# Optimization experiments

Measured on AMD Instinct MI355X. Metric: run time of the kernel, lower is better.

## Reference

```python
import jax, jax.numpy as jnp
import numpy as np

D_LOW = 32
LAGS = [1, 2, 4, 8]
# Upper-triangular pair indices (offset=1), matching torch.triu_indices(d_low, d_low, 1)
IDX_I, IDX_J = np.triu_indices(D_LOW, k=1)
IDX_I = jnp.asarray(IDX_I)
IDX_J = jnp.asarray(IDX_J)
EPS = 1e-6


def setup_inputs() -> dict:
    key = jax.random.key(0)
    ks = jax.random.split(key, 7)
    b, n, d_model = 4, 4096, 1024
    d_plucker = D_LOW * (D_LOW - 1) // 2  # 496
    s = lambda fan_in: 1.0 / np.sqrt(fan_in)
    return {
        "x": jax.random.normal(ks[0], (b, n, d_model), dtype=jnp.float32),
        "W_red": jax.random.normal(ks[1], (d_model, D_LOW), dtype=jnp.float32) * s(d_model),
        "b_red": jax.random.normal(ks[2], (D_LOW,), dtype=jnp.float32) * s(d_model),
        "W_exp": jax.random.normal(ks[3], (d_plucker, d_model), dtype=jnp.float32) * s(d_plucker),
        "b_exp": jax.random.normal(ks[4], (d_model,), dtype=jnp.float32) * s(d_plucker),
        "W_gate": jax.random.normal(ks[5], (2 * d_model, d_model), dtype=jnp.float32) * s(2 * d_model),
        "b_gate": jax.random.normal(ks[6], (d_model,), dtype=jnp.float32) * s(2 * d_model),
    }


def reference(x, W_red, b_red, W_exp, b_exp, W_gate, b_gate):
    b, n, _ = x.shape
    d_plucker = D_LOW * (D_LOW - 1) // 2
    z = x @ W_red + b_red  # [b, n, d_low]
    plucker_total = jnp.zeros((b, n, d_plucker), dtype=x.dtype)
    counts = jnp.zeros((b, n, 1), dtype=x.dtype)
    for lag in LAGS:
        if lag <= 0 or lag >= n:
            continue
        z_curr = z[:, lag:, :]   # [b, n-lag, d_low]
        z_past = z[:, :-lag, :]  # [b, n-lag, d_low]
        # Antisymmetric Plucker coordinates over upper-triangular index pairs
        p = (z_curr[:, :, IDX_I] * z_past[:, :, IDX_J]
             - z_curr[:, :, IDX_J] * z_past[:, :, IDX_I])  # [b, n-lag, d_plucker]
        norm = jnp.linalg.norm(p, axis=-1, keepdims=True)
        p = p / jnp.maximum(norm, EPS)
        plucker_total = plucker_total.at[:, lag:, :].add(p)
        counts = counts.at[:, lag:, :].add(1.0)
    counts = jnp.maximum(counts, 1.0)
    plucker_avg = plucker_total / counts
    g_avg = plucker_avg @ W_exp + b_exp  # [b, n, d_model]
    concat = jnp.concatenate([x, g_avg], axis=-1)  # [b, n, 2*d_model]
    gate = jax.nn.sigmoid(concat @ W_gate + b_gate)
    return gate * x + (1.0 - gate) * g_avg
```

## Files before the change

kernel.cpp:

```cpp
#include <hip/hip_runtime.h>
#include <hip/hip_bf16.h>
#include <math.h>

#define B_DIM   4
#define N_DIM   4096
#define D_MODEL 1024
#define D_LOW   32
#define NPAIR   496
#define NROWS   (B_DIM * N_DIM)
#define KPAD3   512
#define LDA2    1536

typedef __bf16 bf16;
typedef __bf16 bf16x8 __attribute__((ext_vector_type(8)));
typedef __bf16 bf16x4 __attribute__((ext_vector_type(4)));
typedef float  f32x4  __attribute__((ext_vector_type(4)));

#define GLOAD_LDS16(g, l) __builtin_amdgcn_global_load_lds( \
    (__attribute__((address_space(1))) void*)(g),           \
    (__attribute__((address_space(3))) void*)(l), 16, 0, 0)

__global__ __launch_bounds__(256) void wred_t(const float* __restrict__ Wr,
                                              bf16* __restrict__ WrT) {
    __shared__ float tile[32][33];
    const int t  = threadIdx.x;
    const int kb = blockIdx.x * 32;
    {
        int k = t >> 3, c4 = (t & 7) * 4;
        float4 v = *reinterpret_cast<const float4*>(&Wr[(size_t)(kb + k) * 32 + c4]);
        tile[k][c4 + 0] = v.x; tile[k][c4 + 1] = v.y;
        tile[k][c4 + 2] = v.z; tile[k][c4 + 3] = v.w;
    }
    __syncthreads();
    {
        int c = t >> 3, kq = (t & 7) * 4;
        bf16x4 o = { (bf16)tile[kq + 0][c], (bf16)tile[kq + 1][c],
                     (bf16)tile[kq + 2][c], (bf16)tile[kq + 3][c] };
        *reinterpret_cast<bf16x4*>(&WrT[(size_t)c * 1024 + kb + kq]) = o;
    }
}

__global__ __launch_bounds__(256) void k1_mfma(const float* __restrict__ x,
                                               const bf16* __restrict__ WrT,
                                               bf16* __restrict__ a2,
                                               float* __restrict__ zpart) {
    const int t    = threadIdx.x;
    const int wv   = t >> 6, lane = t & 63;
    const int l15  = lane & 15, lhi = lane >> 4;
    const int kc   = blockIdx.x;
    const int mt   = blockIdx.y;
    const int row  = mt * 64 + wv * 16 + l15;
    const int kb   = kc * 512;

    f32x4 accz[2] = { (f32x4){0.f,0.f,0.f,0.f}, (f32x4){0.f,0.f,0.f,0.f} };

#pragma unroll
    for (int ks = 0; ks < 16; ++ks) {
        const int k0 = kb + ks * 32 + lhi * 8;
        const float4 u0 = *reinterpret_cast<const float4*>(&x[(size_t)row * 1024 + k0]);
        const float4 u1 = *reinterpret_cast<const float4*>(&x[(size_t)row * 1024 + k0 + 4]);
        bf16x8 af = { (bf16)u0.x, (bf16)u0.y, (bf16)u0.z, (bf16)u0.w,
                      (bf16)u1.x, (bf16)u1.y, (bf16)u1.z, (bf16)u1.w };
        *reinterpret_cast<bf16x8*>(&a2[(size_t)row * LDA2 + k0]) = af;
        const bf16x8 b0 = *reinterpret_cast<const bf16x8*>(
            &WrT[(size_t)l15 * 1024 + kb + ks * 32 + lhi * 8]);
        const bf16x8 b1 = *reinterpret_cast<const bf16x8*>(
            &WrT[(size_t)(16 + l15) * 1024 + kb + ks * 32 + lhi * 8]);
        accz[0] = __builtin_amdgcn_mfma_f32_16x16x32_bf16(af, b0, accz[0], 0, 0, 0);
        accz[1] = __builtin_amdgcn_mfma_f32_16x16x32_bf16(af, b1, accz[1], 0, 0, 0);
    }
#pragma unroll
    for (int cg = 0; cg < 2; ++cg)
#pragma unroll
        for (int r = 0; r < 4; ++r) {
            const int rout = mt * 64 + wv * 16 + lhi * 4 + r;
            zpart[((size_t)kc * NROWS + rout) * 32 + cg * 16 + l15] = accz[cg][r];
        }
}

__global__ __launch_bounds__(256) void k2_plucker(const float* __restrict__ zpart,
                                                  const float* __restrict__ br,
                                                  bf16* __restrict__ a2) {
    const int wv   = threadIdx.x >> 6;
    const int lane = threadIdx.x & 63;
    const int row  = blockIdx.x * 4 + wv;
    const int t    = row & (N_DIM - 1);
    const int c    = lane & 31;
    const float bias = br[c];

    float zc = bias;
#pragma unroll
    for (int p = 0; p < 2; ++p)
        zc += zpart[((size_t)p * NROWS + row) * 32 + c];

    float zp[4];
    float red[9];
    red[0] = zc * zc;
#pragma unroll
    for (int li = 0; li < 4; ++li) {
        const int lag = 1 << li;
        float v = 0.f;
        if (t >= lag) {
            v = bias;
#pragma unroll
            for (int p = 0; p < 2; ++p)
                v += zpart[((size_t)p * NROWS + (row - lag)) * 32 + c];
        }
        zp[li] = v;
        red[1 + li] = zc * zp[li];
        red[5 + li] = zp[li] * zp[li];
    }
#pragma unroll
    for (int m = 1; m < 32; m <<= 1) {
#pragma unroll
        for (int i = 0; i < 9; ++i) red[i] += __shfl_xor(red[i], m);
    }
    float cnt = 0.f;
#pragma unroll
    for (int li = 0; li < 4; ++li) cnt += (t >= (1 << li)) ? 1.f : 0.f;
    const float inv = 1.f / fmaxf(cnt, 1.f);

    float w = 0.f;
#pragma unroll
    for (int li = 0; li < 4; ++li) {
        float n2 = fmaxf(red[0] * red[5 + li] - red[1 + li] * red[1 + li], 0.f);
        float nr = sqrtf(n2);
        float s  = (t >= (1 << li)) ? inv / fmaxf(nr, 1e-6f) : 0.f;
        w += s * zp[li];
    }

#pragma unroll
    for (int u = 0; u < 8; ++u) {
        const int k = u * 64 + lane;
        float v = 0.f;
        if (k < NPAIR) {
            int kk = k, i = 0;
            while (kk >= 31 - i) { kk -= 31 - i; ++i; }
            const int j = i + 1 + kk;
            float zci = __shfl(zc, i), zcj = __shfl(zc, j);
            float wi  = __shfl(w, i),  wj  = __shfl(w, j);
            v = zci * wj - zcj * wi;
        }
        a2[(size_t)row * LDA2 + 1024 + k] = (bf16)v;
    }
}

__global__ __launch_bounds__(256) void transpose_cvt(const float* __restrict__ src,
                                                     bf16* __restrict__ dst,
                                                     int Ksrc, int Kpad) {
    __shared__ float tile[32][36];
    const int t  = threadIdx.x;
    const int kb = blockIdx.x * 32;
    const int nb = blockIdx.y * 32;
    int li = t * 4;
    int kl = li >> 5, nl = li & 31;
    float4 v = {0.f, 0.f, 0.f, 0.f};
    if (kb + kl < Ksrc)
        v = *reinterpret_cast<const float4*>(&src[(size_t)(kb + kl) * 1024 + nb + nl]);
    tile[kl][nl + 0] = v.x; tile[kl][nl + 1] = v.y;
    tile[kl][nl + 2] = v.z; tile[kl][nl + 3] = v.w;
    __syncthreads();
    int nl2 = li >> 5, kl2 = li & 31;
    bf16x4 o = { (bf16)tile[kl2 + 0][nl2], (bf16)tile[kl2 + 1][nl2],
                 (bf16)tile[kl2 + 2][nl2], (bf16)tile[kl2 + 3][nl2] };
    *reinterpret_cast<bf16x4*>(&dst[(size_t)(nb + nl2) * Kpad + kb + kl2]) = o;
}

__global__ __launch_bounds__(256) void we_cvt_be(const float* __restrict__ We,
                                                 const float* __restrict__ be,
                                                 bf16* __restrict__ WeB) {
    size_t o = ((size_t)blockIdx.x * 256 + threadIdx.x) * 4;
    int row = (int)(o >> 10), col = (int)(o & 1023);
    float4 v = {0.f, 0.f, 0.f, 0.f};
    if (row < NPAIR)      v = *reinterpret_cast<const float4*>(&We[(size_t)row * 1024 + col]);
    else if (row == NPAIR) v = *reinterpret_cast<const float4*>(&be[col]);
    bf16x4 b = { (bf16)v.x, (bf16)v.y, (bf16)v.z, (bf16)v.w };
    *reinterpret_cast<bf16x4*>(&WeB[o]) = b;
}

__global__ __launch_bounds__(256) void wcomb_mfma(const bf16* __restrict__ A,
                                                  const bf16* __restrict__ Bt,
                                                  bf16* __restrict__ BcT) {
    __shared__ bf16 As[128 * 32];
    __shared__ bf16 Bs[128 * 32];
    const int t    = threadIdx.x;
    const int mb   = blockIdx.y * 128;
    const int nbq  = blockIdx.x * 128;
    const int w    = t >> 6, lane = t & 63;
    const int wr   = w >> 1, wc = w & 1;
    const int l15  = lane & 15, lhi = lane >> 4;

    f32x4 acc[4][4];
#pragma unroll
    for (int mt = 0; mt < 4; ++mt)
#pragma unroll
        for (int nt = 0; nt < 4; ++nt) acc[mt][nt] = (f32x4){0.f, 0.f, 0.f, 0.f};

    const int li0 = t, li1 = t + 256;
    const int r0 = li0 >> 2, c0 = (li0 & 3) * 8;
    const int r1 = li1 >> 2, c1 = (li1 & 3) * 8;

    for (int kb = 0; kb < 1024; kb += 32) {
        GLOAD_LDS16(A  + (size_t)(mb + r0) * 1024 + kb + c0, As + li0 * 8);
        GLOAD_LDS16(A  + (size_t)(mb + r1) * 1024 + kb + c1, As + li1 * 8);
        GLOAD_LDS16(Bt + (size_t)(nbq + r0) * 1024 + kb + c0, Bs + li0 * 8);
        GLOAD_LDS16(Bt + (size_t)(nbq + r1) * 1024 + kb + c1, Bs + li1 * 8);
        __syncthreads();
        bf16x8 a[4], b[4];
#pragma unroll
        for (int mt = 0; mt < 4; ++mt)
            a[mt] = *reinterpret_cast<const bf16x8*>(
                As + (wr * 64 + mt * 16 + l15) * 32 + lhi * 8);
#pragma unroll
        for (int nt = 0; nt < 4; ++nt)
            b[nt] = *reinterpret_cast<const bf16x8*>(
                Bs + (wc * 64 + nt * 16 + l15) * 32 + lhi * 8);
#pragma unroll
        for (int mt = 0; mt < 4; ++mt)
#pragma unroll
            for (int nt = 0; nt < 4; ++nt)
                acc[mt][nt] = __builtin_amdgcn_mfma_f32_16x16x32_bf16(
                    a[mt], b[nt], acc[mt][nt], 0, 0, 0);
        __syncthreads();
    }
#pragma unroll
    for (int mt = 0; mt < 4; ++mt)
#pragma unroll
        for (int nt = 0; nt < 4; ++nt) {
            const int col = nbq + wc * 64 + nt * 16 + l15;
#pragma unroll
            for (int r = 0; r < 4; ++r) {
                const int row = mb + wr * 64 + mt * 16 + lhi * 4 + r;
                BcT[(size_t)row * 1536 + 1024 + col] = (bf16)acc[mt][nt][r];
            }
        }
}

__global__ __launch_bounds__(256) void bgc_extract(const float* __restrict__ bg,
                                                   const bf16* __restrict__ BcT,
                                                   float* __restrict__ bgc) {
    int n = blockIdx.x * 256 + threadIdx.x;
    bgc[n] = bg[n] + (float)BcT[(size_t)n * 1536 + 1024 + NPAIR];
}

template <int KDIM, int LDAp, int LDBp, bool GATE>
__global__ __launch_bounds__(512, 2) void gemm8p(const bf16* __restrict__ A,
                                                 const bf16* __restrict__ Bt,
                                                 const float* __restrict__ bias,
                                                 const bf16* __restrict__ gsrc,
                                                 bf16* __restrict__ gdst,
                                                 float* __restrict__ out) {
    extern __shared__ char lds[];
    const int t    = threadIdx.x;
    const int w    = t >> 6, lane = t & 63;
    const int wr   = w >> 2, wc = w & 3;
    const int l15  = lane & 15, lhi = lane >> 4;

    const int fid = blockIdx.x;
    const int xcd = fid & 7, loc = fid >> 3;
    const int mb  = (xcd * 8 + (loc >> 2)) * 256;
    const int nb  = (loc & 3) * 256;

    const int srow = t >> 3;
    const int scol = ((t & 7) ^ (srow & 7)) * 8;
    const size_t aOff = (size_t)(mb + srow) * LDAp + scol;
    const size_t bOff = (size_t)(nb + srow) * LDBp + scol;
    char* const ldsA = lds;
    char* const ldsB = lds + 65536;

#define STAGE_A(d, h, kb) do { \
    GLOAD_LDS16(A + aOff + (size_t)((h) * 128) * LDAp + (kb),      ldsA + (d) * 32768 + (h) * 16384 + t * 16); \
    GLOAD_LDS16(A + aOff + (size_t)((h) * 128 + 64) * LDAp + (kb), ldsA + (d) * 32768 + (h) * 16384 + 8192 + t * 16); } while (0)
#define STAGE_B(d, h, kb) do { \
    GLOAD_LDS16(Bt + bOff + (size_t)((h) * 128) * LDBp + (kb),      ldsB + (d) * 32768 + (h) * 16384 + t * 16); \
    GLOAD_LDS16(Bt + bOff + (size_t)((h) * 128 + 64) * LDBp + (kb), ldsB + (d) * 32768 + (h) * 16384 + 8192 + t * 16); } while (0)

    const int swx = (l15 & 7) << 4;
#define LDAF(d, mq_) do { const char* Ab_ = ldsA + (d) * 32768 + wr * 16384; \
    _Pragma("unroll") for (int mf = 0; mf < 4; ++mf) \
    _Pragma("unroll") for (int ks = 0; ks < 2; ++ks) { \
        int lin = ((mq_) * 64 + mf * 16 + l15) * 128 + ks * 64 + lhi * 16; \
        afr[mf][ks] = *reinterpret_cast<const bf16x8*>(Ab_ + (lin ^ swx)); } } while (0)
#define LDBF(d, nq_) do { const char* Bb_ = ldsB + (d) * 32768 + (wc >> 1) * 16384; \
    _Pragma("unroll") for (int nf = 0; nf < 2; ++nf) \
    _Pragma("unroll") for (int ks = 0; ks < 2; ++ks) { \
        int lin = ((wc & 1) * 64 + (nq_) * 32 + nf * 16 + l15) * 128 + ks * 64 + lhi * 16; \
        bfr[nf][ks] = *reinterpret_cast<const bf16x8*>(Bb_ + (lin ^ swx)); } } while (0)
#define MMA(mq_, nq_) do { __builtin_amdgcn_s_setprio(1); \
    _Pragma("unroll") for (int mf = 0; mf < 4; ++mf) \
    _Pragma("unroll") for (int nf = 0; nf < 2; ++nf) \
    _Pragma("unroll") for (int ks = 0; ks < 2; ++ks) \
        acc[(mq_) * 4 + mf][(nq_) * 2 + nf] = __builtin_amdgcn_mfma_f32_16x16x32_bf16( \
            afr[mf][ks], bfr[nf][ks], acc[(mq_) * 4 + mf][(nq_) * 2 + nf], 0, 0, 0); \
    __builtin_amdgcn_s_setprio(0); } while (0)
#define BAR() asm volatile("s_barrier" ::: "memory")

    f32x4 acc[8][4];
#pragma unroll
    for (int i = 0; i < 8; ++i)
#pragma unroll
        for (int j = 0; j < 4; ++j) acc[i][j] = (f32x4){0.f, 0.f, 0.f, 0.f};
    bf16x8 afr[4][2], bfr[2][2];

    STAGE_B(0, 0, 0); STAGE_B(0, 1, 0);
    STAGE_A(0, 0, 0); STAGE_A(0, 1, 0);
    STAGE_B(1, 0, 64);
    asm volatile("s_waitcnt vmcnt(2)" ::: "memory");
    BAR();

    const int NT    = KDIM / 64;
    const int ITERS = NT / 2;
    for (int it = 0; it < ITERS; ++it) {
        const int k1e = (it * 2 + 1) * 64;
        const int k2e = (it * 2 + 2) * 64;
        const int k3e = (it * 2 + 3) * 64;
        const bool s2 = (it * 2 + 2) < NT;
        const bool s3 = (it * 2 + 3) < NT;
        const bool lastit = (it == ITERS - 1);

        STAGE_B(1, 1, k1e); STAGE_A(1, 0, k1e);
        LDAF(0, 0); LDBF(0, 0);
        BAR(); MMA(0, 0); BAR();
        STAGE_A(1, 1, k1e);
        LDAF(0, 1);
        BAR(); MMA(1, 0); BAR();
        LDBF(0, 1);
        BAR(); MMA(1, 1); BAR();
        if (s2) STAGE_B(0, 0, k2e);
        LDAF(0, 0);
        BAR(); MMA(0, 1);
        if (lastit) asm volatile("s_waitcnt vmcnt(0)" ::: "memory");
        else        asm volatile("s_waitcnt vmcnt(2)" ::: "memory");
        BAR();

        if (s2) { STAGE_B(0, 1, k2e); STAGE_A(0, 0, k2e); }
        LDAF(1, 0); LDBF(1, 0);
        BAR(); MMA(0, 0); BAR();
        if (s2) STAGE_A(0, 1, k2e);
        LDAF(1, 1);
        BAR(); MMA(1, 0); BAR();
        LDBF(1, 1);
        BAR(); MMA(1, 1); BAR();
        if (s3) STAGE_B(1, 0, k3e);
        LDAF(1, 0);
        BAR(); MMA(0, 1);
        if (lastit) asm volatile("s_waitcnt vmcnt(0)" ::: "memory");
        else        asm volatile("s_waitcnt vmcnt(2)" ::: "memory");
        BAR();
    }
#undef STAGE_A
#undef STAGE_B
#undef LDAF
#undef LDBF
#undef MMA
#undef BAR

#pragma unroll
    for (int mi = 0; mi < 8; ++mi) {
#pragma unroll
        for (int nf = 0; nf < 4; ++nf) {
            const int col = nb + wc * 64 + nf * 16 + l15;
            const float bv = bias[col];
#pragma unroll
            for (int r = 0; r < 4; ++r) {
                const int row = mb + wr * 128 + mi * 16 + lhi * 4 + r;
                float v = acc[mi][nf][r] + bv;
                if constexpr (GATE) {
                    float gate = 1.f / (1.f + expf(-v));
                    float xv = (float)A[(size_t)row * LDAp + col];
                    float gv = (float)gsrc[(size_t)row * D_MODEL + col];
                    out[(size_t)row * D_MODEL + col] = gate * xv + (1.f - gate) * gv;
                } else {
                    gdst[(size_t)row * D_MODEL + col] = (bf16)v;
                }
            }
        }
    }
}

extern "C" void kernel_launch(void* const* d_in, const int* in_sizes, int n_in,
                              void* d_out, int out_size, void* d_ws, size_t ws_size,
                              hipStream_t stream) {
    const float* x  = (const float*)d_in[0];
    const float* Wr = (const float*)d_in[1];
    const float* br = (const float*)d_in[2];
    const float* We = (const float*)d_in[3];
    const float* be = (const float*)d_in[4];
    const float* Wg = (const float*)d_in[5];
    const float* bg = (const float*)d_in[6];
    float* out = (float*)d_out;

    char* ws = (char*)d_ws;
    bf16*  gbuf  = (bf16*)(ws);
    float* zpart = (float*)(ws);
    bf16*  A2    = (bf16*)(ws + (32u << 20));
    bf16*  WeT   = (bf16*)(ws + (80u << 20));
    bf16*  BcT   = (bf16*)(ws + (81u << 20));
    bf16*  WgbT  = (bf16*)(ws + (84u << 20));
    bf16*  WeB   = (bf16*)(ws + (86u << 20));
    float* bgc   = (float*)(ws + (87u << 20));
    bf16*  WrT   = (bf16*)(ws + (88u << 20));

    (void)hipFuncSetAttribute(reinterpret_cast<const void*>(&gemm8p<KPAD3, LDA2, KPAD3, false>),
                              hipFuncAttributeMaxDynamicSharedMemorySize, 131072);
    (void)hipFuncSetAttribute(reinterpret_cast<const void*>(&gemm8p<1536, LDA2, 1536, true>),
                              hipFuncAttributeMaxDynamicSharedMemorySize, 131072);

    wred_t<<<32, 256, 0, stream>>>(Wr, WrT);
    k1_mfma<<<dim3(2, 256), 256, 0, stream>>>(x, WrT, A2, zpart);
    k2_plucker<<<NROWS / 4, 256, 0, stream>>>(zpart, br, A2);

    transpose_cvt<<<dim3(KPAD3 / 32, 1024 / 32), 256, 0, stream>>>(We, WeT, NPAIR, KPAD3);
    transpose_cvt<<<dim3(1024 / 32, 1024 / 32), 256, 0, stream>>>(Wg, BcT, 1024, 1536);
    transpose_cvt<<<dim3(1024 / 32, 1024 / 32), 256, 0, stream>>>(Wg + (size_t)1024 * 1024, WgbT, 1024, 1024);
    we_cvt_be<<<512, 256, 0, stream>>>(We, be, WeB);
    wcomb_mfma<<<dim3(4, 8), 256, 0, stream>>>(WgbT, WeB, BcT);
    bgc_extract<<<4, 256, 0, stream>>>(bg, BcT, bgc);

    gemm8p<KPAD3, LDA2, KPAD3, false><<<256, 512, 131072, stream>>>(
        A2 + 1024, WeT, be, nullptr, gbuf, nullptr);
    gemm8p<1536, LDA2, 1536, true><<<256, 512, 131072, stream>>>(
        A2, BcT, bgc, gbuf, nullptr, out);
}
```

Baseline: 165.9 us.

## Replace 8-phase interleaved GEMM pipeline with simple double-buffered K loop

Swaps the hand-interleaved 8-phase schedule, which staged half-tiles of A and B between barrier-separated MFMA groups, for a plain double-buffered loop. Each iteration prefetches the next full K tile into the other LDS buffer, waits on the current tile's loads, then runs the four MMA quadrants with no barriers between them. This cuts barrier count and setprio ping-pong, but loses the fine-grained overlap of global loads with compute across waves and may expose memory latency.

```diff
diff --git a/kernel.cpp b/kernel.cpp
--- a/kernel.cpp
+++ b/kernel.cpp
@@ -244,7 +244,7 @@
 }
 
 template <int KDIM, int LDAp, int LDBp, bool GATE>
-__global__ __launch_bounds__(512, 2) void gemm8p(const bf16* __restrict__ A,
+__global__ __launch_bounds__(512, 2) void gemm2b(const bf16* __restrict__ A,
                                                  const bf16* __restrict__ Bt,
                                                  const float* __restrict__ bias,
                                                  const bf16* __restrict__ gsrc,
@@ -302,51 +302,33 @@
         for (int j = 0; j < 4; ++j) acc[i][j] = (f32x4){0.f, 0.f, 0.f, 0.f};
     bf16x8 afr[4][2], bfr[2][2];
 
+    STAGE_A(0, 0, 0); STAGE_A(0, 1, 0);
     STAGE_B(0, 0, 0); STAGE_B(0, 1, 0);
-    STAGE_A(0, 0, 0); STAGE_A(0, 1, 0);
-    STAGE_B(1, 0, 64);
-    asm volatile("s_waitcnt vmcnt(2)" ::: "memory");
-    BAR();
-
-    const int NT    = KDIM / 64;
-    const int ITERS = NT / 2;
-    for (int it = 0; it < ITERS; ++it) {
-        const int k1e = (it * 2 + 1) * 64;
-        const int k2e = (it * 2 + 2) * 64;
-        const int k3e = (it * 2 + 3) * 64;
-        const bool s2 = (it * 2 + 2) < NT;
-        const bool s3 = (it * 2 + 3) < NT;
-        const bool lastit = (it == ITERS - 1);
-
-        STAGE_B(1, 1, k1e); STAGE_A(1, 0, k1e);
-        LDAF(0, 0); LDBF(0, 0);
-        BAR(); MMA(0, 0); BAR();
-        STAGE_A(1, 1, k1e);
-        LDAF(0, 1);
-        BAR(); MMA(1, 0); BAR();
-        LDBF(0, 1);
-        BAR(); MMA(1, 1); BAR();
-        if (s2) STAGE_B(0, 0, k2e);
-        LDAF(0, 0);
-        BAR(); MMA(0, 1);
-        if (lastit) asm volatile("s_waitcnt vmcnt(0)" ::: "memory");
-        else        asm volatile("s_waitcnt vmcnt(2)" ::: "memory");
+
+    const int NT = KDIM / 64;
+    for (int kt = 0; kt < NT; ++kt) {
+        const int d  = kt & 1;
+        const int kn = (kt + 1) * 64;
+        const bool pre = (kt + 1 < NT);
+
         BAR();
-
-        if (s2) { STAGE_B(0, 1, k2e); STAGE_A(0, 0, k2e); }
-        LDAF(1, 0); LDBF(1, 0);
-        BAR(); MMA(0, 0); BAR();
-        if (s2) STAGE_A(0, 1, k2e);
-        LDAF(1, 1);
-        BAR(); MMA(1, 0); BAR();
-        LDBF(1, 1);
-        BAR(); MMA(1, 1); BAR();
-        if (s3) STAGE_B(1, 0, k3e);
-        LDAF(1, 0);
-        BAR(); MMA(0, 1);
-        if (lastit) asm volatile("s_waitcnt vmcnt(0)" ::: "memory");
-        else        asm volatile("s_waitcnt vmcnt(2)" ::: "memory");
+        if (pre) {
+            STAGE_A(d ^ 1, 0, kn); STAGE_A(d ^ 1, 1, kn);
+            STAGE_B(d ^ 1, 0, kn); STAGE_B(d ^ 1, 1, kn);
+            asm volatile("s_waitcnt vmcnt(8)" ::: "memory");
+        } else {
+            asm volatile("s_waitcnt vmcnt(0)" ::: "memory");
+        }
         BAR();
+
+        LDAF(d, 0); LDBF(d, 0);
+        MMA(0, 0);
+        LDAF(d, 1);
+        MMA(1, 0);
+        LDBF(d, 1);
+        MMA(1, 1);
+        LDAF(d, 0);
+        MMA(0, 1);
     }
 #undef STAGE_A
 #undef STAGE_B
@@ -401,9 +383,9 @@
     float* bgc   = (float*)(ws + (87u << 20));
     bf16*  WrT   = (bf16*)(ws + (88u << 20));
 
-    (void)hipFuncSetAttribute(reinterpret_cast<const void*>(&gemm8p<KPAD3, LDA2, KPAD3, false>),
+    (void)hipFuncSetAttribute(reinterpret_cast<const void*>(&gemm2b<KPAD3, LDA2, KPAD3, false>),
                               hipFuncAttributeMaxDynamicSharedMemorySize, 131072);
-    (void)hipFuncSetAttribute(reinterpret_cast<const void*>(&gemm8p<1536, LDA2, 1536, true>),
+    (void)hipFuncSetAttribute(reinterpret_cast<const void*>(&gemm2b<1536, LDA2, 1536, true>),
                               hipFuncAttributeMaxDynamicSharedMemorySize, 131072);
 
     wred_t<<<32, 256, 0, stream>>>(Wr, WrT);
@@ -417,8 +399,8 @@
     wcomb_mfma<<<dim3(4, 8), 256, 0, stream>>>(WgbT, WeB, BcT);
     bgc_extract<<<4, 256, 0, stream>>>(bg, BcT, bgc);
 
-    gemm8p<KPAD3, LDA2, KPAD3, false><<<256, 512, 131072, stream>>>(
+    gemm2b<KPAD3, LDA2, KPAD3, false><<<256, 512, 131072, stream>>>(
         A2 + 1024, WeT, be, nullptr, gbuf, nullptr);
-    gemm8p<1536, LDA2, 1536, true><<<256, 512, 131072, stream>>>(
+    gemm2b<1536, LDA2, 1536, true><<<256, 512, 131072, stream>>>(
         A2, BcT, bgc, gbuf, nullptr, out);
 }
```

Measured after the change: 169.4 us. +2.1%, slower.
